# Performance work log

Hardware: AMD Instinct MI355X
Metric: run time of the kernel (lower is better)

Reference implementation:

```python
import jax, jax.numpy as jnp
import numpy as np

MARGIN = 0.5
POS_WEIGHT = 0.5
NEG_WEIGHT = 0.5
PUNISHMENT_SCALE = 2.0
POS_THRESHOLD = 0.6
NEG_THRESHOLD = 0.3
BIG = 1e9  # finite sentinel instead of inf (grad-safe under where)


def setup_inputs() -> dict:
    key = jax.random.key(0)
    k1, k2, k3 = jax.random.split(key, 3)
    N, D = 8192, 256
    embeddings = jax.random.normal(k1, (N, D), dtype=jnp.float32)
    labels = jax.random.randint(k2, (N,), 0, 2, dtype=jnp.int32)
    pids = jax.random.randint(k3, (N,), 0, 256, dtype=jnp.int32)
    return {"embeddings": embeddings, "labels": labels, "pids": pids}


def reference(embeddings, labels, pids):
    N = embeddings.shape[0]
    # F.normalize(p=2, dim=1): x / max(||x||, eps)
    norm = jnp.maximum(jnp.linalg.norm(embeddings, axis=1, keepdims=True), 1e-12)
    normed = embeddings / norm
    sim = normed @ normed.T  # (N, N) cosine similarity

    same_pid = pids[:, None] == pids[None, :]            # (N, N)
    genuine_j = (labels == 1)[None, :]                   # (1, N)
    not_self = ~jnp.eye(N, dtype=bool)
    pos_mask = same_pid & genuine_j & not_self           # same pid, genuine, not anchor
    neg_mask = (same_pid & ~genuine_j) | ~same_pid       # same-pid forgeries or cross-pid

    valid = (labels == 1) & pos_mask.any(axis=1) & neg_mask.any(axis=1)

    # hardest positive = min similarity among positives
    hp = jnp.min(jnp.where(pos_mask, sim, BIG), axis=1)  # (N,)

    # semi-hard negatives: hp - margin < sim < hp
    semi = neg_mask & (sim < hp[:, None]) & (sim > (hp - MARGIN)[:, None])
    cand = neg_mask & (sim > hp[:, None])                # harder-than-positive negatives
    hn_semi = jnp.max(jnp.where(semi, sim, -BIG), axis=1)
    hn_cand = jnp.max(jnp.where(cand, sim, -BIG), axis=1)
    hn_all = jnp.max(jnp.where(neg_mask, sim, -BIG), axis=1)
    hn = jnp.where(semi.any(axis=1), hn_semi,
                   jnp.where(cand.any(axis=1), hn_cand, hn_all))

    base = jax.nn.relu(hn - hp + MARGIN)
    weight = jnp.where((hp < POS_THRESHOLD) | (hn > NEG_THRESHOLD),
                       PUNISHMENT_SCALE, 1.0)
    loss = base * weight + POS_WEIGHT * (1.0 - hp) + NEG_WEIGHT * jax.nn.relu(hn + 0.2)

    cnt = jnp.sum(valid)
    total = jnp.sum(jnp.where(valid, loss, 0.0))
    return jnp.where(cnt > 0, total / jnp.maximum(cnt, 1), 0.0)
```

## Files before the change

kernel.cpp:

```cpp
#include <hip/hip_runtime.h>
#include <hip/hip_bf16.h>
#include <stdint.h>

typedef __attribute__((ext_vector_type(8))) short short8;
typedef __attribute__((ext_vector_type(4))) float f32x4;

#define BIGF 1e9f
#define NSLOT 16
#define MAXM 96

__device__ inline float blo(unsigned int u) {
    union { unsigned int i; float f; } v; v.i = u << 16; return v.f;
}
__device__ inline float bhi(unsigned int u) {
    union { unsigned int i; float f; } v; v.i = u & 0xffff0000u; return v.f;
}
__device__ inline unsigned int fkey(float s) {
    unsigned int b = __float_as_uint(s);
    return (b & 0x80000000u) ? ~b : (b | 0x80000000u);
}
__device__ inline float funkey(unsigned int k) {
    unsigned int b = (k & 0x80000000u) ? (k & 0x7fffffffu) : ~k;
    return __uint_as_float(b);
}
__device__ inline void async16(const unsigned short* g, unsigned short* l) {
    __builtin_amdgcn_global_load_lds(
        (const __attribute__((address_space(1))) void*)g,
        (__attribute__((address_space(3))) void*)l, 16, 0, 0);
}
__device__ inline unsigned short f2b(float x) {
    __hip_bfloat16 h = __float2bfloat16(x);
    return *reinterpret_cast<unsigned short*>(&h);
}

__global__ __launch_bounds__(256) void k_prep(
    const float* __restrict__ emb, const int* __restrict__ labels,
    const int* __restrict__ pids, unsigned short* __restrict__ normed,
    int* __restrict__ gpid, float* __restrict__ hp_out,
    float* __restrict__ gred, int* __restrict__ done, int N)
{
    __shared__ int list[MAXM];
    __shared__ unsigned int hp_loc[MAXM];
    __shared__ unsigned short rows[MAXM * 256];
    __shared__ int cnt;

    const int b = blockIdx.x;
    const int t = threadIdx.x;
    const int nblk = N / 4;
    const int w = t >> 6, lane = t & 63;

    if (b < nblk) {
        if (b == 0 && t < 3) {
            if (t < 2) gred[t] = 0.f;
            else *done = 0;
        }
        int row = b * 4 + w;
        const float4* src = (const float4*)(emb + ((size_t)row << 8));
        float4 x = src[lane];
        float ss = x.x * x.x + x.y * x.y + x.z * x.z + x.w * x.w;
        #pragma unroll
        for (int off = 32; off >= 1; off >>= 1) ss += __shfl_xor(ss, off, 64);
        float inv = 1.0f / fmaxf(sqrtf(ss), 1e-12f);
        ushort4 o;
        o.x = f2b(x.x * inv); o.y = f2b(x.y * inv);
        o.z = f2b(x.z * inv); o.w = f2b(x.w * inv);
        ((ushort4*)(normed + ((size_t)row << 8)))[lane] = o;
        if (lane == 0) {
            int genuine = (labels[row] == 1);
            gpid[row] = genuine ? pids[row] : -1;
            if (!genuine) hp_out[row] = BIGF;
        }
        return;
    }

    int p = b - nblk;
    if (t == 0) cnt = 0;
    __syncthreads();
    for (int j = t; j < N; j += 256)
        if (pids[j] == p && labels[j] == 1) {
            int idx = atomicAdd(&cnt, 1);
            if (idx < MAXM) list[idx] = j;
        }
    __syncthreads();
    int M = min(cnt, MAXM);
    for (int s = t; s < M; s += 256) hp_loc[s] = 0xFFFFFFFFu;
    for (int mi = w; mi < M; mi += 4) {
        const float4* src = (const float4*)(emb + ((size_t)list[mi] << 8));
        float4 x = src[lane];
        float ss = x.x * x.x + x.y * x.y + x.z * x.z + x.w * x.w;
        #pragma unroll
        for (int off = 32; off >= 1; off >>= 1) ss += __shfl_xor(ss, off, 64);
        float inv = 1.0f / fmaxf(sqrtf(ss), 1e-12f);
        ushort4 o;
        o.x = f2b(x.x * inv); o.y = f2b(x.y * inv);
        o.z = f2b(x.z * inv); o.w = f2b(x.w * inv);
        ((ushort4*)&rows[mi * 256])[lane] = o;
    }
    __syncthreads();
    for (int pr = t; pr < M * M; pr += 256) {
        int i = pr / M, j = pr - i * M;
        if (i == j) continue;
        const uint4* ap = (const uint4*)&rows[i * 256];
        const uint4* bp = (const uint4*)&rows[j * 256];
        float s = 0.f;
        #pragma unroll 4
        for (int k = 0; k < 32; ++k) {
            uint4 a = ap[k], bb = bp[k];
            s += blo(a.x) * blo(bb.x) + bhi(a.x) * bhi(bb.x);
            s += blo(a.y) * blo(bb.y) + bhi(a.y) * bhi(bb.y);
            s += blo(a.z) * blo(bb.z) + bhi(a.z) * bhi(bb.z);
            s += blo(a.w) * blo(bb.w) + bhi(a.w) * bhi(bb.w);
        }
        atomicMin(&hp_loc[i], fkey(s));
    }
    __syncthreads();
    for (int s = t; s < M; s += 256) {
        unsigned int key = hp_loc[s];
        hp_out[list[s]] = (key == 0xFFFFFFFFu) ? BIGF : funkey(key);
    }
}

__global__ __launch_bounds__(256, 2) void k_pass2(
    const unsigned short* __restrict__ normed, const int* __restrict__ pids,
    const int* __restrict__ gpid, const float* __restrict__ hp,
    float* __restrict__ p_hn, float* __restrict__ p_mb, int N)
{
    __shared__ unsigned short As[64 * 256];
    __shared__ unsigned short Bs[2][256 * 32];
    __shared__ int pid_s[64];
    __shared__ float hp_s[64];

    const int t = threadIdx.x;
    const int lane = t & 63;
    const int wc = t >> 6;
    const int quad = lane >> 4, l16 = lane & 15;
    const int strip = blockIdx.x >> 2;
    const int split = blockIdx.x & 3;
    const int rbase = strip * 64;
    const int cstart = split * (N >> 2);

    if (t < 64) { pid_s[t] = pids[rbase + t]; hp_s[t] = hp[rbase + t]; }

    #pragma unroll
    for (int i = 0; i < 8; ++i) {
        int C = i * 256 + t;
        int kb = C >> 8, rem = C & 255, row = rem >> 2, pos = rem & 3;
        int c = pos ^ ((row >> 1) & 3);
        async16(normed + ((size_t)(rbase + row) << 8) + kb * 32 + c * 8,
                &As[C * 8]);
    }
    const int bcol[4] = { 0 * 64 + (t >> 2), 1 * 64 + (t >> 2),
                          2 * 64 + (t >> 2), 3 * 64 + (t >> 2) };
    const unsigned short* gB[4];
    #pragma unroll
    for (int i = 0; i < 4; ++i) {
        int c = (t & 3) ^ ((bcol[i] >> 1) & 3);
        gB[i] = normed + ((size_t)(cstart + bcol[i]) << 8) + c * 8;
    }
    #pragma unroll
    for (int i = 0; i < 4; ++i)
        async16(gB[i], &Bs[0][(i * 256 + t) * 8]);

    __syncthreads();

    int pid_c[4][4]; float hp_c[4][4];
    float hnall[4][4], mbel[4][4];
    f32x4 acc[4][4];
    #pragma unroll
    for (int mt = 0; mt < 4; ++mt)
        #pragma unroll
        for (int r = 0; r < 4; ++r) {
            int rl = mt * 16 + quad * 4 + r;
            pid_c[mt][r] = pid_s[rl];
            hp_c[mt][r] = hp_s[rl];
            hnall[mt][r] = -BIGF;
            mbel[mt][r] = -BIGF;
        }
    #pragma unroll
    for (int mt = 0; mt < 4; ++mt)
        #pragma unroll
        for (int nt = 0; nt < 4; ++nt)
            acc[mt][nt] = (f32x4){0.f, 0.f, 0.f, 0.f};

    const int sw = (l16 >> 1) & 3;
    const int aoff = l16 * 32 + (quad ^ sw) * 8;
    int gp[4];

    for (int s = 0; s < 64; ++s) {
        const int ti = s >> 3, kb = s & 7, buf = s & 1;
        if (s < 63) {
            int s1 = s + 1;
            size_t off = ((size_t)(s1 >> 3) << 16) + (size_t)(s1 & 7) * 32;
            #pragma unroll
            for (int i = 0; i < 4; ++i)
                async16(gB[i] + off, &Bs[buf ^ 1][(i * 256 + t) * 8]);
        }
        if (kb == 0) {
            int cb = cstart + ti * 256 + wc * 64;
            #pragma unroll
            for (int nt = 0; nt < 4; ++nt) gp[nt] = gpid[cb + nt * 16 + l16];
        }
        short8 af[4], bf[4];
        #pragma unroll
        for (int mt = 0; mt < 4; ++mt)
            af[mt] = *reinterpret_cast<const short8*>(
                &As[kb * 2048 + mt * 512 + aoff]);
        #pragma unroll
        for (int nt = 0; nt < 4; ++nt)
            bf[nt] = *reinterpret_cast<const short8*>(
                &Bs[buf][wc * 2048 + nt * 512 + aoff]);
        #pragma unroll
        for (int mt = 0; mt < 4; ++mt)
            #pragma unroll
            for (int nt = 0; nt < 4; ++nt)
                acc[mt][nt] = __builtin_amdgcn_mfma_f32_16x16x32_bf16(
                    af[mt], bf[nt], acc[mt][nt], 0, 0, 0);
        if (kb == 7) {
            #pragma unroll
            for (int mt = 0; mt < 4; ++mt)
                #pragma unroll
                for (int r = 0; r < 4; ++r) {
                    int prow = pid_c[mt][r];
                    float hprow = hp_c[mt][r];
                    #pragma unroll
                    for (int nt = 0; nt < 4; ++nt) {
                        float sv = acc[mt][nt][r];
                        float tt = (prow != gp[nt]) ? sv : -BIGF;
                        hnall[mt][r] = fmaxf(hnall[mt][r], tt);
                        float u = (tt < hprow) ? tt : -BIGF;
                        mbel[mt][r] = fmaxf(mbel[mt][r], u);
                        acc[mt][nt][r] = 0.f;
                    }
                }
        }
        __syncthreads();
    }

    #pragma unroll
    for (int mt = 0; mt < 4; ++mt)
        #pragma unroll
        for (int r = 0; r < 4; ++r) {
            float v1 = hnall[mt][r], v2 = mbel[mt][r];
            #pragma unroll
            for (int off = 8; off >= 1; off >>= 1) {
                v1 = fmaxf(v1, __shfl_xor(v1, off, 64));
                v2 = fmaxf(v2, __shfl_xor(v2, off, 64));
            }
            if (l16 == 0) {
                int row = rbase + mt * 16 + quad * 4 + r;
                int slot = split * 4 + wc;
                p_hn[(size_t)slot * N + row] = v1;
                p_mb[(size_t)slot * N + row] = v2;
            }
        }
}

__global__ __launch_bounds__(256) void k_rowloss(
    const float* __restrict__ hp, const float* __restrict__ p_hn,
    const float* __restrict__ p_mb, const int* __restrict__ labels,
    float* __restrict__ gred, int* __restrict__ done,
    float* __restrict__ out, int N)
{
    int i = blockIdx.x * 256 + threadIdx.x;
    float hn_all = -BIGF, mb = -BIGF;
    #pragma unroll
    for (int s = 0; s < NSLOT; ++s) {
        hn_all = fmaxf(hn_all, p_hn[(size_t)s * N + i]);
        mb = fmaxf(mb, p_mb[(size_t)s * N + i]);
    }
    float hpv = hp[i];
    bool valid = (labels[i] == 1) && (hpv < 1e8f) && (hn_all > -1e8f);
    float hn = (mb > hpv - 0.5f) ? mb : hn_all;
    float base = fmaxf(hn - hpv + 0.5f, 0.f);
    float wgt = (hpv < 0.6f || hn > 0.3f) ? 2.f : 1.f;
    float loss = base * wgt + 0.5f * (1.f - hpv) + 0.5f * fmaxf(hn + 0.2f, 0.f);
    float lsum = valid ? loss : 0.f;
    float lcnt = valid ? 1.f : 0.f;
    #pragma unroll
    for (int off = 32; off >= 1; off >>= 1) {
        lsum += __shfl_xor(lsum, off, 64);
        lcnt += __shfl_xor(lcnt, off, 64);
    }
    __shared__ float rs[4], rc[4];
    int wv = threadIdx.x >> 6, lane = threadIdx.x & 63;
    if (lane == 0) { rs[wv] = lsum; rc[wv] = lcnt; }
    __syncthreads();
    if (threadIdx.x == 0) {
        atomicAdd(&gred[0], rs[0] + rs[1] + rs[2] + rs[3]);
        atomicAdd(&gred[1], rc[0] + rc[1] + rc[2] + rc[3]);
        __threadfence();
        int old = atomicAdd(done, 1);
        if (old == (int)gridDim.x - 1) {
            float S = atomicAdd(&gred[0], 0.f);
            float C = atomicAdd(&gred[1], 0.f);
            out[0] = (C > 0.f) ? S / fmaxf(C, 1.f) : 0.f;
        }
    }
}

extern "C" void kernel_launch(void* const* d_in, const int* in_sizes, int n_in,
                              void* d_out, int out_size, void* d_ws, size_t ws_size,
                              hipStream_t stream)
{
    const float* emb = (const float*)d_in[0];
    const int* labels = (const int*)d_in[1];
    const int* pids = (const int*)d_in[2];
    float* out = (float*)d_out;
    int N = in_sizes[1];

    char* ws = (char*)d_ws;
    unsigned short* normed = (unsigned short*)ws;  ws += (size_t)N * 256 * 2;
    int* gpid = (int*)ws;                          ws += (size_t)N * 4;
    float* hp = (float*)ws;                        ws += (size_t)N * 4;
    float* p_hn = (float*)ws;                      ws += (size_t)N * NSLOT * 4;
    float* p_mb = (float*)ws;                      ws += (size_t)N * NSLOT * 4;
    float* gred = (float*)ws;                      ws += 2 * 4;
    int* done = (int*)ws;                          ws += 4;

    k_prep<<<N / 4 + 256, 256, 0, stream>>>(emb, labels, pids, normed, gpid,
                                            hp, gred, done, N);
    k_pass2<<<(N / 64) * 4, 256, 0, stream>>>(normed, pids, gpid, hp,
                                              p_hn, p_mb, N);
    k_rowloss<<<N / 256, 256, 0, stream>>>(hp, p_hn, p_mb, labels,
                                           gred, done, out, N);
}
```

Baseline: 150.2 us.

## Load B fragments directly from global into registers, drop shared B buffer and barrier

Replaces the double-buffered shared-memory staging of B column tiles in pass2 with direct per-lane global loads into registers, prefetched two steps ahead. This removes the shared-memory B buffers and the per-step __syncthreads, cutting barrier stalls and LDS traffic. In exchange each wave issues its own uncoalesced-ish 16-byte global loads (no sharing across waves) and register pressure rises from the prefetch buffers, which may reduce occupancy or expose global latency.

Result: slower. 249.7 us (+66.3%).

```diff
diff --git a/kernel.cpp b/kernel.cpp
--- a/kernel.cpp
+++ b/kernel.cpp
@@ -126,7 +126,6 @@
     float* __restrict__ p_hn, float* __restrict__ p_mb, int N)
 {
     __shared__ unsigned short As[64 * 256];
-    __shared__ unsigned short Bs[2][256 * 32];
     __shared__ int pid_s[64];
     __shared__ float hp_s[64];
 
@@ -149,17 +148,18 @@
         async16(normed + ((size_t)(rbase + row) << 8) + kb * 32 + c * 8,
                 &As[C * 8]);
     }
-    const int bcol[4] = { 0 * 64 + (t >> 2), 1 * 64 + (t >> 2),
-                          2 * 64 + (t >> 2), 3 * 64 + (t >> 2) };
-    const unsigned short* gB[4];
-    #pragma unroll
-    for (int i = 0; i < 4; ++i) {
-        int c = (t & 3) ^ ((bcol[i] >> 1) & 3);
-        gB[i] = normed + ((size_t)(cstart + bcol[i]) << 8) + c * 8;
-    }
-    #pragma unroll
-    for (int i = 0; i < 4; ++i)
-        async16(gB[i], &Bs[0][(i * 256 + t) * 8]);
+
+    const uint4* gB4 = (const uint4*)normed;
+    int base[4];
+    #pragma unroll
+    for (int nt = 0; nt < 4; ++nt)
+        base[nt] = (cstart + wc * 64 + nt * 16 + l16) * 32 + quad;
+
+    uint4 pf[2][4];
+    #pragma unroll
+    for (int nt = 0; nt < 4; ++nt) pf[0][nt] = gB4[base[nt]];
+    #pragma unroll
+    for (int nt = 0; nt < 4; ++nt) pf[1][nt] = gB4[base[nt] + 4];
 
     __syncthreads();
 
@@ -187,28 +187,28 @@
     int gp[4];
 
     for (int s = 0; s < 64; ++s) {
-        const int ti = s >> 3, kb = s & 7, buf = s & 1;
-        if (s < 63) {
-            int s1 = s + 1;
-            size_t off = ((size_t)(s1 >> 3) << 16) + (size_t)(s1 & 7) * 32;
-            #pragma unroll
-            for (int i = 0; i < 4; ++i)
-                async16(gB[i] + off, &Bs[buf ^ 1][(i * 256 + t) * 8]);
-        }
+        const int ti = s >> 3, kb = s & 7, cur = s & 1;
         if (kb == 0) {
             int cb = cstart + ti * 256 + wc * 64;
             #pragma unroll
             for (int nt = 0; nt < 4; ++nt) gp[nt] = gpid[cb + nt * 16 + l16];
         }
-        short8 af[4], bf[4];
+        short8 bf[4];
+        #pragma unroll
+        for (int nt = 0; nt < 4; ++nt)
+            bf[nt] = *reinterpret_cast<const short8*>(&pf[cur][nt]);
+        if (s + 2 < 64) {
+            int s2 = s + 2;
+            int off2 = (s2 >> 3) * 8192 + (s2 & 7) * 4;
+            #pragma unroll
+            for (int nt = 0; nt < 4; ++nt)
+                pf[cur][nt] = gB4[base[nt] + off2];
+        }
+        short8 af[4];
         #pragma unroll
         for (int mt = 0; mt < 4; ++mt)
             af[mt] = *reinterpret_cast<const short8*>(
                 &As[kb * 2048 + mt * 512 + aoff]);
-        #pragma unroll
-        for (int nt = 0; nt < 4; ++nt)
-            bf[nt] = *reinterpret_cast<const short8*>(
-                &Bs[buf][wc * 2048 + nt * 512 + aoff]);
         #pragma unroll
         for (int mt = 0; mt < 4; ++mt)
             #pragma unroll
@@ -233,7 +233,6 @@
                     }
                 }
         }
-        __syncthreads();
     }
 
     #pragma unroll
```
